# Performance work log

Measured on AMD Instinct MI355X. Metric: run time of the kernel, lower is better.

Reference implementation:

```python
import jax, jax.numpy as jnp
import numpy as np

N = 10000          # variable nodes
DEG = 16           # average degree
F = N * DEG // 2   # factors (80000)
E = 2 * F          # directed edges per direction (160000)
S = 64             # state_dim
M = 64             # message_dim
HM = 128           # hidden_unit_message_dim
HR = 128           # hidden_unit_readout_dim
STEPS = 5          # n_steps


def setup_inputs() -> dict:
    rng = np.random.default_rng(0)
    u = rng.integers(0, N - 1, size=F)
    v = u + 1 + rng.integers(0, N - 1 - u)          # u < v, factor endpoints
    b = rng.standard_normal(N).astype(np.float32)
    Juv = rng.standard_normal(F).astype(np.float32)
    pair = np.stack([u, v], axis=1).reshape(-1)      # [E] node endpoints (u,v interleaved)
    fidx = np.repeat(np.arange(F), 2)                # [E] factor index, each twice
    base = np.stack([np.zeros(F, np.float32), b[u].astype(np.float32),
                     b[v].astype(np.float32), Juv], axis=1)   # [F,4]
    base2 = np.repeat(base, 2, axis=0)               # [E,4]
    v2f_feat = base2.copy()                          # flag 0.0
    f2v_feat = base2.copy(); f2v_feat[:, 0] = 1.0    # flag 1.0

    keys = jax.random.split(jax.random.key(0), 32)
    p = lambda k, shp: (jax.random.normal(k, shp, jnp.float32) * 0.1)
    z = lambda n: jnp.zeros((n,), jnp.float32)
    inp = {
        'fac2var_row': jnp.asarray(fidx, jnp.int32),
        'fac2var_col': jnp.asarray(pair, jnp.int32),
        'var2fac_row': jnp.asarray(pair, jnp.int32),
        'var2fac_col': jnp.asarray(fidx, jnp.int32),
        'fac2var_feat': jnp.asarray(f2v_feat),
        'var2fac_feat': jnp.asarray(v2f_feat),
        # fac2var message MLP (in = 2S+8)
        'f2v_w1': p(keys[0], (HM, 2 * S + 8)), 'f2v_b1': z(HM),
        'f2v_w2': p(keys[1], (HM, HM)),        'f2v_b2': z(HM),
        'f2v_w3': p(keys[2], (M, HM)),         'f2v_b3': z(M),
        # var2fac message MLP
        'v2f_w1': p(keys[3], (HM, 2 * S + 8)), 'v2f_b1': z(HM),
        'v2f_w2': p(keys[4], (HM, HM)),        'v2f_b2': z(HM),
        'v2f_w3': p(keys[5], (M, HM)),         'v2f_b3': z(M),
        # fac2var GRUCell (input M, hidden S)
        'gf_wih': p(keys[6], (3 * S, M)), 'gf_whh': p(keys[7], (3 * S, S)),
        'gf_bih': p(keys[8], (3 * S,)),   'gf_bhh': p(keys[9], (3 * S,)),
        # var2fac GRUCell
        'gv_wih': p(keys[10], (3 * S, M)), 'gv_whh': p(keys[11], (3 * S, S)),
        'gv_bih': p(keys[12], (3 * S,)),   'gv_bhh': p(keys[13], (3 * S,)),
        # readout MLP
        'ro_w1': p(keys[14], (HR, S)),  'ro_b1': z(HR),
        'ro_w2': p(keys[15], (HR, HR)), 'ro_b2': z(HR),
        'ro_w3': p(keys[16], (2, HR)),  'ro_b3': z(2),
    }
    return inp


def _mlp3(x, w1, b1, w2, b2, w3, b3):
    h = jax.nn.relu(x @ w1.T + b1)
    h = jax.nn.relu(h @ w2.T + b2)
    return h @ w3.T + b3


def _gru(x, h, wih, whh, bih, bhh):
    gi = x @ wih.T + bih
    gh = h @ whh.T + bhh
    ir, iz, inn = jnp.split(gi, 3, axis=-1)
    hr, hz, hn = jnp.split(gh, 3, axis=-1)
    r = jax.nn.sigmoid(ir + hr)
    zg = jax.nn.sigmoid(iz + hz)
    n = jnp.tanh(inn + r * hn)
    return (1.0 - zg) * n + zg * h


def reference(fac2var_row, fac2var_col, var2fac_row, var2fac_col,
              fac2var_feat, var2fac_feat,
              f2v_w1, f2v_b1, f2v_w2, f2v_b2, f2v_w3, f2v_b3,
              v2f_w1, v2f_b1, v2f_w2, v2f_b2, v2f_w3, v2f_b3,
              gf_wih, gf_whh, gf_bih, gf_bhh,
              gv_wih, gv_whh, gv_bih, gv_bhh,
              ro_w1, ro_b1, ro_w2, ro_b2, ro_w3, ro_b3):
    var_h0 = jnp.zeros((N, S), jnp.float32)
    fac_h0 = jnp.zeros((F, S), jnp.float32)

    def step(carry, _):
        var_h, fac_h = carry
        # fac -> var
        em = jnp.concatenate([fac_h[fac2var_row], var_h[fac2var_col],
                              fac2var_feat[fac2var_row], fac2var_feat[fac2var_col]], axis=-1)
        em = _mlp3(em, f2v_w1, f2v_b1, f2v_w2, f2v_b2, f2v_w3, f2v_b3)
        nm = jax.ops.segment_sum(em, fac2var_col, num_segments=N)
        var_h = _gru(nm, var_h, gf_wih, gf_whh, gf_bih, gf_bhh)
        # var -> fac
        em = jnp.concatenate([var_h[var2fac_row], fac_h[var2fac_col],
                              var2fac_feat[var2fac_row], var2fac_feat[var2fac_col]], axis=-1)
        em = _mlp3(em, v2f_w1, v2f_b1, v2f_w2, v2f_b2, v2f_w3, v2f_b3)
        nm = jax.ops.segment_sum(em, var2fac_col, num_segments=F)
        fac_h = _gru(nm, fac_h, gv_wih, gv_whh, gv_bih, gv_bhh)
        return (var_h, fac_h), None

    (var_h, _), _ = jax.lax.scan(step, (var_h0, fac_h0), None, length=STEPS)
    logits = _mlp3(var_h, ro_w1, ro_b1, ro_w2, ro_b2, ro_w3, ro_b3)
    return jax.nn.softmax(logits, axis=1)
```

## Files before the change

### kernel.cpp

```cpp
#include <hip/hip_runtime.h>
#include <hip/hip_bf16.h>

#define NN     10000
#define NF     80000
#define NE     160000
#define SDIM   64
#define HMDIM  128
#define HRDIM  128
#define KIN    136
#define NSTEPS 5

static_assert(NE % 64 == 0, "edge grid exact");

typedef __attribute__((ext_vector_type(8))) short short8;
typedef __attribute__((ext_vector_type(4))) float f32x4;

static __device__ __forceinline__ float bf2f(unsigned short u) {
    return __uint_as_float(((unsigned int)u) << 16);
}
static __device__ __forceinline__ unsigned short f2bf(float f) {
    __hip_bfloat16 h = __float2bfloat16(f);
    unsigned short u;
    __builtin_memcpy(&u, &h, 2);
    return u;
}
static __device__ __forceinline__ float sigm(float x) {
    x = fminf(fmaxf(x, -30.f), 30.f);
    return 1.f / (1.f + __expf(-x));
}
static __device__ __forceinline__ float tanh_f(float x) {
    x = fminf(fmaxf(x, -15.f), 15.f);
    float t = __expf(2.f * x);
    return (t - 1.f) / (t + 1.f);
}
static __device__ __forceinline__ void split8(const float* x, short8& hi, short8& lo) {
    #pragma unroll
    for (int i = 0; i < 8; ++i) {
        unsigned short h = f2bf(x[i]);
        hi[i] = (short)h;
        lo[i] = (short)f2bf(x[i] - bf2f(h));
    }
}
static __device__ __forceinline__ void f4pair_to8(float4 a, float4 b, float* xv) {
    xv[0]=a.x; xv[1]=a.y; xv[2]=a.z; xv[3]=a.w;
    xv[4]=b.x; xv[5]=b.y; xv[6]=b.z; xv[7]=b.w;
}
static __device__ __forceinline__ void dma16(const unsigned short* g, unsigned short* l) {
    __builtin_amdgcn_global_load_lds(
        (const __attribute__((address_space(1))) void*)g,
        (__attribute__((address_space(3))) void*)l,
        16, 0, 0);
}

#define LGKM0() asm volatile("s_waitcnt lgkmcnt(0)" ::: "memory")
#define VMC2()  asm volatile("s_waitcnt vmcnt(2)"   ::: "memory")
#define VMC0()  asm volatile("s_waitcnt vmcnt(0)"   ::: "memory")
#define SBAR()  __builtin_amdgcn_s_barrier()
#define SCHED0() __builtin_amdgcn_sched_barrier(0)
#define PRIO1() __builtin_amdgcn_s_setprio(1)
#define PRIO0() __builtin_amdgcn_s_setprio(0)

__global__ void k_zero(float* __restrict__ p, int n) {
    int i = blockIdx.x * blockDim.x + threadIdx.x;
    int stride = gridDim.x * blockDim.x;
    for (; i < n; i += stride) p[i] = 0.f;
}

#define NTR 2
struct TArgs {
    const float* src[NTR];
    float*       dst[NTR];
    int          R[NTR];
    int          C[NTR];
};
__global__ void k_transpose(TArgs a) {
    const int b = blockIdx.x;
    const float* s = a.src[b];
    float* d = a.dst[b];
    const int R = a.R[b], C = a.C[b], n = R * C;
    for (int i = threadIdx.x; i < n; i += blockDim.x) {
        int r = i / C, c = i % C;
        d[c * R + r] = s[i];
    }
}

#define NPK 10
struct PArgs {
    const float*    src[NPK];
    unsigned short* hi[NPK];
    unsigned short* lo[NPK];
    int             N[NPK], K[NPK], CK[NPK];
};
__global__ void k_pack(PArgs a) {
    const int b = blockIdx.x;
    const float* s = a.src[b];
    unsigned short* ph = a.hi[b];
    unsigned short* pl = a.lo[b];
    const int N = a.N[b], K = a.K[b], CK = a.CK[b];
    const int NT = N >> 4;
    const int total = NT * CK * 512;
    for (int i = threadIdx.x; i < total; i += blockDim.x) {
        int j    = i & 7;
        int ln   = (i >> 3) & 63;
        int tile = i >> 9;
        int tn   = tile % NT;
        int ck   = tile / NT;
        int k = ck * 32 + ((ln >> 4) * 8) + j;
        int n = tn * 16 + (ln & 15);
        float f = (k < K) ? s[n * K + k] : 0.f;
        unsigned short h = f2bf(f);
        ph[i] = h;
        pl[i] = f2bf(f - bf2f(h));
    }
}

__global__ void k_bsum(const float* bih0, const float* bhh0, float* o0,
                       const float* bih1, const float* bhh1, float* o1) {
    int i = threadIdx.x;
    if (i < 192) { o0[i] = bih0[i] + bhh0[i]; o1[i] = bih1[i] + bhh1[i]; }
}

#define STAGE(buf, sh, sl) do {                                            \
    const int u0_ = wv * 2;                                                \
    _Pragma("unroll")                                                      \
    for (int k_ = 0; k_ < 2; ++k_) {                                       \
        const int u_ = u0_ + k_;                                           \
        const unsigned short* s_ = (u_ < 4 ? (sh) : (sl)) + (u_ & 3) * 512;\
        unsigned short* d_ = (u_ < 4 ? &BH[buf][0] : &BL[buf][0]) + (u_ & 3) * 512; \
        dma16(s_ + lane * 8, d_);                                          \
    }                                                                      \
} while (0)

__global__ __launch_bounds__(256, 3)
void k_edge_mfma(const float* __restrict__ hrow, const float* __restrict__ hcol,
                 const int* __restrict__ rows, const int* __restrict__ cols,
                 const float* __restrict__ feat,
                 const unsigned short* __restrict__ w1h, const unsigned short* __restrict__ w1l,
                 const unsigned short* __restrict__ w2h, const unsigned short* __restrict__ w2l,
                 const unsigned short* __restrict__ w3h, const unsigned short* __restrict__ w3l,
                 const float* __restrict__ b1, const float* __restrict__ b2,
                 const float* __restrict__ b3,
                 float* __restrict__ nm, int pairsum)
{
    __shared__ __align__(16) unsigned short Hhi[64][136];
    __shared__ __align__(16) unsigned short Hlo[64][136];
    __shared__ __align__(16) unsigned short BH[2][2048];
    __shared__ __align__(16) unsigned short BL[2][2048];
    const int lane = threadIdx.x & 63;
    const int wv   = threadIdx.x >> 6;
    const int quad = lane >> 4;
    const int col  = lane & 15;

    const int e0 = blockIdx.x * 64 + wv * 16 + col;
    const int r0 = pairsum ? rows[e0] : (e0 >> 1);
    const int c0 = pairsum ? (e0 >> 1) : cols[e0];

    float4 gR[4], gC[4], gFr, gFc;
    {
        const float4* pr = (const float4*)(hrow + (size_t)r0 * 64);
        const float4* pc = (const float4*)(hcol + (size_t)c0 * 64);
        gR[0] = pr[quad * 2];     gR[1] = pr[quad * 2 + 1];
        gR[2] = pr[8 + quad * 2]; gR[3] = pr[8 + quad * 2 + 1];
        gC[0] = pc[quad * 2];     gC[1] = pc[quad * 2 + 1];
        gC[2] = pc[8 + quad * 2]; gC[3] = pc[8 + quad * 2 + 1];
        gFr = *(const float4*)(feat + (size_t)r0 * 4);
        gFc = *(const float4*)(feat + (size_t)c0 * 4);
    }
    int cc[4];
    if (!pairsum) {
        #pragma unroll
        for (int rr = 0; rr < 4; ++rr)
            cc[rr] = cols[blockIdx.x * 64 + wv * 16 + quad * 4 + rr];
    }
    float b1v[8], b2v[8], b3v[4];
    #pragma unroll
    for (int t = 0; t < 8; ++t) { b1v[t] = b1[t * 16 + col]; b2v[t] = b2[t * 16 + col]; }
    #pragma unroll
    for (int t = 0; t < 4; ++t) b3v[t] = b3[t * 16 + col];

    VMC0(); SCHED0();

    STAGE(0, w1h, w1l);

    f32x4 acc[8];
    #pragma unroll
    for (int t = 0; t < 8; ++t) acc[t] = (f32x4){0.f, 0.f, 0.f, 0.f};

    short8 ahi, alo;
    #pragma unroll
    for (int hp = 0; hp < 10; ++hp) {
        {
            const unsigned short* nh; const unsigned short* nl;
            if (hp < 9) { nh = w1h + (hp + 1) * 2048; nl = w1l + (hp + 1) * 2048; }
            else        { nh = w2h;                   nl = w2l; }
            STAGE((hp + 1) & 1, nh, nl);
        }
        if ((hp & 1) == 0) {
            const int ck = hp >> 1;
            float xv[8];
            if (ck < 2)      f4pair_to8(gR[ck * 2], gR[ck * 2 + 1], xv);
            else if (ck < 4) f4pair_to8(gC[(ck - 2) * 2], gC[(ck - 2) * 2 + 1], xv);
            else if (quad == 0) f4pair_to8(gFr, gFc, xv);
            else {
                #pragma unroll
                for (int i = 0; i < 8; ++i) xv[i] = 0.f;
            }
            split8(xv, ahi, alo);
        }
        VMC2(); LGKM0(); SBAR(); SCHED0();
        {
            const unsigned short* bh = &BH[hp & 1][0];
            const unsigned short* bl = &BL[hp & 1][0];
            #pragma unroll
            for (int t = 0; t < 4; ++t) {
                const int tn = (hp & 1) * 4 + t;
                short8 bhi = *(const short8*)(bh + t * 512 + lane * 8);
                short8 blo = *(const short8*)(bl + t * 512 + lane * 8);
                acc[tn] = __builtin_amdgcn_mfma_f32_16x16x32_bf16(ahi, bhi, acc[tn], 0, 0, 0);
                acc[tn] = __builtin_amdgcn_mfma_f32_16x16x32_bf16(ahi, blo, acc[tn], 0, 0, 0);
                acc[tn] = __builtin_amdgcn_mfma_f32_16x16x32_bf16(alo, bhi, acc[tn], 0, 0, 0);
            }
        }
        LGKM0(); SBAR(); SCHED0();
    }
    #pragma unroll
    for (int tn = 0; tn < 8; ++tn)
        #pragma unroll
        for (int rr = 0; rr < 4; ++rr) {
            float v = fmaxf(acc[tn][rr] + b1v[tn], 0.f);
            int m = wv * 16 + quad * 4 + rr;
            unsigned short h = f2bf(v);
            Hhi[m][tn * 16 + col] = h;
            Hlo[m][tn * 16 + col] = f2bf(v - bf2f(h));
        }

    #pragma unroll
    for (int t = 0; t < 8; ++t) acc[t] = (f32x4){0.f, 0.f, 0.f, 0.f};
    const int m0 = wv * 16 + col;
    #pragma unroll
    for (int h2 = 0; h2 < 8; ++h2) {
        const int hp = 10 + h2;
        {
            const unsigned short* nh; const unsigned short* nl;
            if (h2 < 7) { nh = w2h + (h2 + 1) * 2048; nl = w2l + (h2 + 1) * 2048; }
            else        { nh = w3h;                   nl = w3l; }
            STAGE((hp + 1) & 1, nh, nl);
        }
        if ((h2 & 1) == 0) {
            const int ck = h2 >> 1;
            ahi = *(const short8*)(&Hhi[m0][ck * 32 + quad * 8]);
            alo = *(const short8*)(&Hlo[m0][ck * 32 + quad * 8]);
        }
        VMC2(); LGKM0(); SBAR(); SCHED0();
        {
            const unsigned short* bh = &BH[hp & 1][0];
            const unsigned short* bl = &BL[hp & 1][0];
            #pragma unroll
            for (int t = 0; t < 4; ++t) {
                const int tn = (h2 & 1) * 4 + t;
                short8 bhi = *(const short8*)(bh + t * 512 + lane * 8);
                short8 blo = *(const short8*)(bl + t * 512 + lane * 8);
                acc[tn] = __builtin_amdgcn_mfma_f32_16x16x32_bf16(ahi, bhi, acc[tn], 0, 0, 0);
                acc[tn] = __builtin_amdgcn_mfma_f32_16x16x32_bf16(ahi, blo, acc[tn], 0, 0, 0);
                acc[tn] = __builtin_amdgcn_mfma_f32_16x16x32_bf16(alo, bhi, acc[tn], 0, 0, 0);
            }
        }
        LGKM0(); SBAR(); SCHED0();
    }
    #pragma unroll
    for (int tn = 0; tn < 8; ++tn)
        #pragma unroll
        for (int rr = 0; rr < 4; ++rr) {
            float v = fmaxf(acc[tn][rr] + b2v[tn], 0.f);
            int m = wv * 16 + quad * 4 + rr;
            unsigned short h = f2bf(v);
            Hhi[m][tn * 16 + col] = h;
            Hlo[m][tn * 16 + col] = f2bf(v - bf2f(h));
        }

    f32x4 a3[4];
    #pragma unroll
    for (int t = 0; t < 4; ++t) a3[t] = (f32x4){0.f, 0.f, 0.f, 0.f};
    #pragma unroll
    for (int h3 = 0; h3 < 4; ++h3) {
        const int hp = 18 + h3;
        if (h3 < 3) STAGE((hp + 1) & 1, w3h + (h3 + 1) * 2048, w3l + (h3 + 1) * 2048);
        short8 a3h = *(const short8*)(&Hhi[m0][h3 * 32 + quad * 8]);
        short8 a3l = *(const short8*)(&Hlo[m0][h3 * 32 + quad * 8]);
        if (h3 < 3) { VMC2(); } else { VMC0(); }
        LGKM0(); SBAR(); SCHED0();
        {
            const unsigned short* bh = &BH[hp & 1][0];
            const unsigned short* bl = &BL[hp & 1][0];
            #pragma unroll
            for (int t = 0; t < 4; ++t) {
                short8 bhi = *(const short8*)(bh + t * 512 + lane * 8);
                short8 blo = *(const short8*)(bl + t * 512 + lane * 8);
                a3[t] = __builtin_amdgcn_mfma_f32_16x16x32_bf16(a3h, bhi, a3[t], 0, 0, 0);
                a3[t] = __builtin_amdgcn_mfma_f32_16x16x32_bf16(a3h, blo, a3[t], 0, 0, 0);
                a3[t] = __builtin_amdgcn_mfma_f32_16x16x32_bf16(a3l, bhi, a3[t], 0, 0, 0);
            }
        }
        if (h3 < 3) { LGKM0(); SBAR(); SCHED0(); }
    }

    if (pairsum) {
        int f0 = (blockIdx.x * 64 + wv * 16 + quad * 4) >> 1;
        #pragma unroll
        for (int tn = 0; tn < 4; ++tn) {
            float b2x = 2.f * b3v[tn];
            nm[(size_t)f0 * 64 + tn * 16 + col]       = a3[tn][0] + a3[tn][1] + b2x;
            nm[(size_t)(f0 + 1) * 64 + tn * 16 + col] = a3[tn][2] + a3[tn][3] + b2x;
        }
    } else {
        #pragma unroll
        for (int tn = 0; tn < 4; ++tn) {
            float bias = b3v[tn];
            #pragma unroll
            for (int rr = 0; rr < 4; ++rr)
                atomicAdd(&nm[(size_t)cc[rr] * 64 + tn * 16 + col], a3[tn][rr] + bias);
        }
    }
}

__global__ __launch_bounds__(256, 3)
void k_gru_mfma(float* __restrict__ nm,
                const unsigned short* __restrict__ wih_h, const unsigned short* __restrict__ wih_l,
                const unsigned short* __restrict__ whh_h, const unsigned short* __restrict__ whh_l,
                const float* __restrict__ bsum,
                const float* __restrict__ bih, const float* __restrict__ bhh,
                float* __restrict__ hst, int count, int nzero)
{
    __shared__ float Hs[64][68];
    const int lane = threadIdx.x & 63;
    const int wv   = threadIdx.x >> 6;
    const int quad = lane >> 4;
    const int col  = lane & 15;
    const int base = blockIdx.x * 64;

    float4 am[4], ah[4];
    {
        int ra = base + wv * 16 + col;
        ra = ra < count ? ra : count - 1;
        const float4* pm = (const float4*)(nm + (size_t)ra * 64);
        const float4* ph = (const float4*)(hst + (size_t)ra * 64);
        am[0] = pm[quad * 2];     am[1] = pm[quad * 2 + 1];
        am[2] = pm[8 + quad * 2]; am[3] = pm[8 + quad * 2 + 1];
        ah[0] = ph[quad * 2];     ah[1] = ph[quad * 2 + 1];
        ah[2] = ph[8 + quad * 2]; ah[3] = ph[8 + quad * 2 + 1];
    }
    float bsr[4], bsz[4], bin_[4], bhn[4];
    #pragma unroll
    for (int t = 0; t < 4; ++t) {
        int g = t * 16 + col;
        bsr[t] = bsum[g]; bsz[t] = bsum[64 + g];
        bin_[t] = bih[128 + g]; bhn[t] = bhh[128 + g];
    }
    {
        int rowl = wv * 16 + col;
        *(float4*)(&Hs[rowl][quad * 8])          = ah[0];
        *(float4*)(&Hs[rowl][quad * 8 + 4])      = ah[1];
        *(float4*)(&Hs[rowl][32 + quad * 8])     = ah[2];
        *(float4*)(&Hs[rowl][32 + quad * 8 + 4]) = ah[3];
    }

    f32x4 rz[8], ni[4], nh[4];
    #pragma unroll
    for (int t = 0; t < 8; ++t) rz[t] = (f32x4){0.f, 0.f, 0.f, 0.f};
    #pragma unroll
    for (int t = 0; t < 4; ++t) {
        ni[t] = (f32x4){0.f, 0.f, 0.f, 0.f};
        nh[t] = (f32x4){0.f, 0.f, 0.f, 0.f};
    }

    #pragma unroll
    for (int ck = 0; ck < 2; ++ck) {
        short8 mhi, mlo, hhi, hlo;
        {
            float xv[8];
            f4pair_to8(am[ck * 2], am[ck * 2 + 1], xv);
            split8(xv, mhi, mlo);
            f4pair_to8(ah[ck * 2], ah[ck * 2 + 1], xv);
            split8(xv, hhi, hlo);
        }
        const unsigned short* ih = wih_h + (size_t)(ck * 12) * 512 + lane * 8;
        const unsigned short* il = wih_l + (size_t)(ck * 12) * 512 + lane * 8;
        const unsigned short* hh = whh_h + (size_t)(ck * 12) * 512 + lane * 8;
        const unsigned short* hl = whh_l + (size_t)(ck * 12) * 512 + lane * 8;
        PRIO1();
        #pragma unroll
        for (int tn = 0; tn < 8; ++tn) {
            short8 bihh = *(const short8*)(ih + tn * 512);
            short8 bihl = *(const short8*)(il + tn * 512);
            short8 bhhh = *(const short8*)(hh + tn * 512);
            short8 bhhl = *(const short8*)(hl + tn * 512);
            rz[tn] = __builtin_amdgcn_mfma_f32_16x16x32_bf16(mhi, bihh, rz[tn], 0, 0, 0);
            rz[tn] = __builtin_amdgcn_mfma_f32_16x16x32_bf16(mhi, bihl, rz[tn], 0, 0, 0);
            rz[tn] = __builtin_amdgcn_mfma_f32_16x16x32_bf16(mlo, bihh, rz[tn], 0, 0, 0);
            rz[tn] = __builtin_amdgcn_mfma_f32_16x16x32_bf16(hhi, bhhh, rz[tn], 0, 0, 0);
            rz[tn] = __builtin_amdgcn_mfma_f32_16x16x32_bf16(hhi, bhhl, rz[tn], 0, 0, 0);
            rz[tn] = __builtin_amdgcn_mfma_f32_16x16x32_bf16(hlo, bhhh, rz[tn], 0, 0, 0);
        }
        #pragma unroll
        for (int tn = 8; tn < 12; ++tn) {
            short8 bihh = *(const short8*)(ih + tn * 512);
            short8 bihl = *(const short8*)(il + tn * 512);
            short8 bhhh = *(const short8*)(hh + tn * 512);
            short8 bhhl = *(const short8*)(hl + tn * 512);
            ni[tn - 8] = __builtin_amdgcn_mfma_f32_16x16x32_bf16(mhi, bihh, ni[tn - 8], 0, 0, 0);
            ni[tn - 8] = __builtin_amdgcn_mfma_f32_16x16x32_bf16(mhi, bihl, ni[tn - 8], 0, 0, 0);
            ni[tn - 8] = __builtin_amdgcn_mfma_f32_16x16x32_bf16(mlo, bihh, ni[tn - 8], 0, 0, 0);
            nh[tn - 8] = __builtin_amdgcn_mfma_f32_16x16x32_bf16(hhi, bhhh, nh[tn - 8], 0, 0, 0);
            nh[tn - 8] = __builtin_amdgcn_mfma_f32_16x16x32_bf16(hhi, bhhl, nh[tn - 8], 0, 0, 0);
            nh[tn - 8] = __builtin_amdgcn_mfma_f32_16x16x32_bf16(hlo, bhhh, nh[tn - 8], 0, 0, 0);
        }
        PRIO0();
    }

    #pragma unroll
    for (int rr = 0; rr < 4; ++rr) {
        int rowl = wv * 16 + quad * 4 + rr;
        int grow = base + rowl;
        bool ok = grow < count;
        #pragma unroll
        for (int t = 0; t < 4; ++t) {
            int g = t * 16 + col;
            float rv = sigm(rz[t][rr] + bsr[t]);
            float zv = sigm(rz[4 + t][rr] + bsz[t]);
            float nv = tanh_f(ni[t][rr] + bin_[t] + rv * (nh[t][rr] + bhn[t]));
            if (ok) {
                float ho = Hs[rowl][g];
                hst[(size_t)grow * 64 + g] = (1.f - zv) * nv + zv * ho;
            }
            if (grow < nzero) nm[(size_t)grow * 64 + g] = 0.f;
        }
    }
}

__global__ __launch_bounds__(256, 3)
void k_readout(const float* __restrict__ vh,
               const float* __restrict__ w1t, const float* __restrict__ b1,
               const float* __restrict__ w2t, const float* __restrict__ b2,
               const float* __restrict__ w3, const float* __restrict__ b3,
               float* __restrict__ out)
{
    __shared__ float H[HRDIM][64];
    const int lane = threadIdx.x & 63;
    const int wv   = __builtin_amdgcn_readfirstlane(threadIdx.x >> 6);
    const int n0 = blockIdx.x * 64 + lane;
    const int n  = n0 < NN ? n0 : NN - 1;
    const float4* px = (const float4*)(vh + (size_t)n * 64);

    const int j1 = 32 * wv;
    float acc[32];
    #pragma unroll
    for (int j = 0; j < 32; ++j) acc[j] = b1[j1 + j];
    #pragma unroll 4
    for (int q = 0; q < 16; ++q) {
        float4 x4 = px[q];
        const float* wa = w1t + (4 * q + 0) * HRDIM + j1;
        const float* wb = w1t + (4 * q + 1) * HRDIM + j1;
        const float* wc = w1t + (4 * q + 2) * HRDIM + j1;
        const float* wd = w1t + (4 * q + 3) * HRDIM + j1;
        #pragma unroll
        for (int j = 0; j < 32; ++j) {
            acc[j] = fmaf(wa[j], x4.x, acc[j]);
            acc[j] = fmaf(wb[j], x4.y, acc[j]);
            acc[j] = fmaf(wc[j], x4.z, acc[j]);
            acc[j] = fmaf(wd[j], x4.w, acc[j]);
        }
    }
    #pragma unroll
    for (int j = 0; j < 32; ++j) H[j1 + j][lane] = fmaxf(acc[j], 0.f);
    __syncthreads();

    #pragma unroll
    for (int j = 0; j < 32; ++j) acc[j] = b2[j1 + j];
    #pragma unroll 4
    for (int k = 0; k < HRDIM; ++k) {
        float xk = H[k][lane];
        const float* wr = w2t + k * HRDIM + j1;
        #pragma unroll
        for (int j = 0; j < 32; ++j)
            acc[j] = fmaf(wr[j], xk, acc[j]);
    }
    __syncthreads();
    #pragma unroll
    for (int j = 0; j < 32; ++j) H[j1 + j][lane] = fmaxf(acc[j], 0.f);
    __syncthreads();

    if (wv == 0 && n0 < NN) {
        float l0 = b3[0], l1 = b3[1];
        #pragma unroll 8
        for (int k = 0; k < HRDIM; ++k) {
            float hk = H[k][lane];
            l0 = fmaf(w3[k],         hk, l0);
            l1 = fmaf(w3[HRDIM + k], hk, l1);
        }
        float mx = fmaxf(l0, l1);
        float e0 = __expf(l0 - mx), e1 = __expf(l1 - mx);
        float inv = 1.f / (e0 + e1);
        out[2 * n + 0] = e0 * inv;
        out[2 * n + 1] = e1 * inv;
    }
}

extern "C" void kernel_launch(void* const* d_in, const int* in_sizes, int n_in,
                              void* d_out, int out_size, void* d_ws, size_t ws_size,
                              hipStream_t stream)
{
    float* var_h = (float*)d_ws;
    float* fac_h = var_h + 640000;
    float* nm    = fac_h + 5120000;
    float* ro_t  = nm + 5120000;
    float* bsum  = ro_t + 24576;
    unsigned short* pk = (unsigned short*)(bsum + 384);

    const int*   f2v_row  = (const int*)d_in[0];
    const int*   f2v_col  = (const int*)d_in[1];
    const int*   v2f_row  = (const int*)d_in[2];
    const int*   v2f_col  = (const int*)d_in[3];
    const float* f2v_feat = (const float*)d_in[4];
    const float* v2f_feat = (const float*)d_in[5];
    const float* W[26];
    for (int j = 0; j < 26; ++j) W[j] = (const float*)d_in[6 + j];

    TArgs ta;
    float* T[NTR];
    {
        const float* src[NTR] = { W[20], W[22] };
        int R[NTR] = { HRDIM, HRDIM };
        int C[NTR] = { SDIM, HRDIM };
        size_t off = 0;
        for (int t = 0; t < NTR; ++t) {
            ta.src[t] = src[t]; ta.R[t] = R[t]; ta.C[t] = C[t];
            T[t] = ro_t + off; ta.dst[t] = T[t];
            off += (size_t)R[t] * C[t];
        }
    }
    unsigned short* P[12];
    unsigned short* G[8];
    {
        size_t off = 0;
        int esz[3] = { 20480, 16384, 8192 };
        for (int d = 0; d < 2; ++d)
            for (int m = 0; m < 3; ++m) {
                P[d * 6 + m * 2 + 0] = pk + off; off += esz[m];
                P[d * 6 + m * 2 + 1] = pk + off; off += esz[m];
            }
        for (int t = 0; t < 8; ++t) { G[t] = pk + off; off += 12288; }
    }
    PArgs pa;
    {
        const float* src[NPK] = { W[0], W[2], W[4], W[6], W[8], W[10],
                                  W[12], W[13], W[16], W[17] };
        int N[NPK]  = { HMDIM, HMDIM, SDIM,  HMDIM, HMDIM, SDIM,  192, 192, 192, 192 };
        int K[NPK]  = { KIN,   HMDIM, HMDIM, KIN,   HMDIM, HMDIM, SDIM, SDIM, SDIM, SDIM };
        int CK[NPK] = { 5,     4,     4,     5,     4,     4,     2,   2,   2,   2 };
        unsigned short* hi[NPK] = { P[0], P[2], P[4], P[6], P[8], P[10],
                                    G[0], G[2], G[4], G[6] };
        unsigned short* lo[NPK] = { P[1], P[3], P[5], P[7], P[9], P[11],
                                    G[1], G[3], G[5], G[7] };
        for (int t = 0; t < NPK; ++t) {
            pa.src[t] = src[t]; pa.N[t] = N[t]; pa.K[t] = K[t]; pa.CK[t] = CK[t];
            pa.hi[t] = hi[t];   pa.lo[t] = lo[t];
        }
    }
    k_transpose<<<NTR, 256, 0, stream>>>(ta);
    k_pack<<<NPK, 256, 0, stream>>>(pa);
    k_bsum<<<1, 256, 0, stream>>>(W[14], W[15], bsum, W[18], W[19], bsum + 192);
    k_zero<<<512, 256, 0, stream>>>(var_h, 640000 + 5120000 + 5120000);

    for (int s = 0; s < NSTEPS; ++s) {
        k_edge_mfma<<<NE / 64, 256, 0, stream>>>(
            fac_h, var_h, f2v_row, f2v_col, f2v_feat,
            P[0], P[1], P[2], P[3], P[4], P[5],
            W[1], W[3], W[5], nm, 0);
        k_gru_mfma<<<(NN + 63) / 64, 256, 0, stream>>>(
            nm, G[0], G[1], G[2], G[3], bsum, W[14], W[15], var_h, NN, 0);
        k_edge_mfma<<<NE / 64, 256, 0, stream>>>(
            var_h, fac_h, v2f_row, v2f_col, v2f_feat,
            P[6], P[7], P[8], P[9], P[10], P[11],
            W[7], W[9], W[11], nm, 1);
        k_gru_mfma<<<(NF + 63) / 64, 256, 0, stream>>>(
            nm, G[4], G[5], G[6], G[7], bsum + 192, W[18], W[19], fac_h, NF, NN);
    }
    k_readout<<<(NN + 63) / 64, 256, 0, stream>>>(
        var_h, T[0], W[21], T[1], W[23], W[24], W[25],
        (float*)d_out);
}
```

Measured before the change: 1.035 ms.

## Load MLP weight fragments directly from global instead of LDS-staged DMA pipeline

Removes the double-buffered global-to-LDS DMA staging of weight tiles, along with its per-chunk waitcnt and barrier synchronisation. Each wave now reads its bf16 hi/lo weight fragments straight from global memory, relying on L1/L2 caching because the weights are small and shared. This frees LDS and drops block barriers, and the occupancy hint rises from 3 to 4 blocks per CU. The cost is redundant per-wave global or cache traffic for weights and exposed load latency before each MFMA.

```diff
diff --git a/kernel.cpp b/kernel.cpp
--- a/kernel.cpp
+++ b/kernel.cpp
@@ -45,18 +45,7 @@
     xv[0]=a.x; xv[1]=a.y; xv[2]=a.z; xv[3]=a.w;
     xv[4]=b.x; xv[5]=b.y; xv[6]=b.z; xv[7]=b.w;
 }
-static __device__ __forceinline__ void dma16(const unsigned short* g, unsigned short* l) {
-    __builtin_amdgcn_global_load_lds(
-        (const __attribute__((address_space(1))) void*)g,
-        (__attribute__((address_space(3))) void*)l,
-        16, 0, 0);
-}
-
-#define LGKM0() asm volatile("s_waitcnt lgkmcnt(0)" ::: "memory")
-#define VMC2()  asm volatile("s_waitcnt vmcnt(2)"   ::: "memory")
-#define VMC0()  asm volatile("s_waitcnt vmcnt(0)"   ::: "memory")
-#define SBAR()  __builtin_amdgcn_s_barrier()
-#define SCHED0() __builtin_amdgcn_sched_barrier(0)
+
 #define PRIO1() __builtin_amdgcn_s_setprio(1)
 #define PRIO0() __builtin_amdgcn_s_setprio(0)
 
@@ -120,18 +109,7 @@
     if (i < 192) { o0[i] = bih0[i] + bhh0[i]; o1[i] = bih1[i] + bhh1[i]; }
 }
 
-#define STAGE(buf, sh, sl) do {                                            \
-    const int u0_ = wv * 2;                                                \
-    _Pragma("unroll")                                                      \
-    for (int k_ = 0; k_ < 2; ++k_) {                                       \
-        const int u_ = u0_ + k_;                                           \
-        const unsigned short* s_ = (u_ < 4 ? (sh) : (sl)) + (u_ & 3) * 512;\
-        unsigned short* d_ = (u_ < 4 ? &BH[buf][0] : &BL[buf][0]) + (u_ & 3) * 512; \
-        dma16(s_ + lane * 8, d_);                                          \
-    }                                                                      \
-} while (0)
-
-__global__ __launch_bounds__(256, 3)
+__global__ __launch_bounds__(256, 4)
 void k_edge_mfma(const float* __restrict__ hrow, const float* __restrict__ hcol,
                  const int* __restrict__ rows, const int* __restrict__ cols,
                  const float* __restrict__ feat,
@@ -144,8 +122,6 @@
 {
     __shared__ __align__(16) unsigned short Hhi[64][136];
     __shared__ __align__(16) unsigned short Hlo[64][136];
-    __shared__ __align__(16) unsigned short BH[2][2048];
-    __shared__ __align__(16) unsigned short BL[2][2048];
     const int lane = threadIdx.x & 63;
     const int wv   = threadIdx.x >> 6;
     const int quad = lane >> 4;
@@ -178,25 +154,16 @@
     #pragma unroll
     for (int t = 0; t < 4; ++t) b3v[t] = b3[t * 16 + col];
 
-    VMC0(); SCHED0();
-
-    STAGE(0, w1h, w1l);
-
     f32x4 acc[8];
     #pragma unroll
     for (int t = 0; t < 8; ++t) acc[t] = (f32x4){0.f, 0.f, 0.f, 0.f};
 
-    short8 ahi, alo;
-    #pragma unroll
-    for (int hp = 0; hp < 10; ++hp) {
+    const int boff = lane * 8;
+
+    #pragma unroll
+    for (int ck = 0; ck < 5; ++ck) {
+        short8 ahi, alo;
         {
-            const unsigned short* nh; const unsigned short* nl;
-            if (hp < 9) { nh = w1h + (hp + 1) * 2048; nl = w1l + (hp + 1) * 2048; }
-            else        { nh = w2h;                   nl = w2l; }
-            STAGE((hp + 1) & 1, nh, nl);
-        }
-        if ((hp & 1) == 0) {
-            const int ck = hp >> 1;
             float xv[8];
             if (ck < 2)      f4pair_to8(gR[ck * 2], gR[ck * 2 + 1], xv);
             else if (ck < 4) f4pair_to8(gC[(ck - 2) * 2], gC[(ck - 2) * 2 + 1], xv);
@@ -207,21 +174,16 @@
             }
             split8(xv, ahi, alo);
         }
-        VMC2(); LGKM0(); SBAR(); SCHED0();
-        {
-            const unsigned short* bh = &BH[hp & 1][0];
-            const unsigned short* bl = &BL[hp & 1][0];
-            #pragma unroll
-            for (int t = 0; t < 4; ++t) {
-                const int tn = (hp & 1) * 4 + t;
-                short8 bhi = *(const short8*)(bh + t * 512 + lane * 8);
-                short8 blo = *(const short8*)(bl + t * 512 + lane * 8);
-                acc[tn] = __builtin_amdgcn_mfma_f32_16x16x32_bf16(ahi, bhi, acc[tn], 0, 0, 0);
-                acc[tn] = __builtin_amdgcn_mfma_f32_16x16x32_bf16(ahi, blo, acc[tn], 0, 0, 0);
-                acc[tn] = __builtin_amdgcn_mfma_f32_16x16x32_bf16(alo, bhi, acc[tn], 0, 0, 0);
-            }
-        }
-        LGKM0(); SBAR(); SCHED0();
+        const unsigned short* bh = w1h + ck * 4096 + boff;
+        const unsigned short* bl = w1l + ck * 4096 + boff;
+        #pragma unroll
+        for (int tn = 0; tn < 8; ++tn) {
+            short8 bhi = *(const short8*)(bh + tn * 512);
+            short8 blo = *(const short8*)(bl + tn * 512);
+            acc[tn] = __builtin_amdgcn_mfma_f32_16x16x32_bf16(ahi, bhi, acc[tn], 0, 0, 0);
+            acc[tn] = __builtin_amdgcn_mfma_f32_16x16x32_bf16(ahi, blo, acc[tn], 0, 0, 0);
+            acc[tn] = __builtin_amdgcn_mfma_f32_16x16x32_bf16(alo, bhi, acc[tn], 0, 0, 0);
+        }
     }
     #pragma unroll
     for (int tn = 0; tn < 8; ++tn)
@@ -238,34 +200,19 @@
     for (int t = 0; t < 8; ++t) acc[t] = (f32x4){0.f, 0.f, 0.f, 0.f};
     const int m0 = wv * 16 + col;
     #pragma unroll
-    for (int h2 = 0; h2 < 8; ++h2) {
-        const int hp = 10 + h2;
-        {
-            const unsigned short* nh; const unsigned short* nl;
-            if (h2 < 7) { nh = w2h + (h2 + 1) * 2048; nl = w2l + (h2 + 1) * 2048; }
-            else        { nh = w3h;                   nl = w3l; }
-            STAGE((hp + 1) & 1, nh, nl);
-        }
-        if ((h2 & 1) == 0) {
-            const int ck = h2 >> 1;
-            ahi = *(const short8*)(&Hhi[m0][ck * 32 + quad * 8]);
-            alo = *(const short8*)(&Hlo[m0][ck * 32 + quad * 8]);
-        }
-        VMC2(); LGKM0(); SBAR(); SCHED0();
-        {
-            const unsigned short* bh = &BH[hp & 1][0];
-            const unsigned short* bl = &BL[hp & 1][0];
-            #pragma unroll
-            for (int t = 0; t < 4; ++t) {
-                const int tn = (h2 & 1) * 4 + t;
-                short8 bhi = *(const short8*)(bh + t * 512 + lane * 8);
-                short8 blo = *(const short8*)(bl + t * 512 + lane * 8);
-                acc[tn] = __builtin_amdgcn_mfma_f32_16x16x32_bf16(ahi, bhi, acc[tn], 0, 0, 0);
-                acc[tn] = __builtin_amdgcn_mfma_f32_16x16x32_bf16(ahi, blo, acc[tn], 0, 0, 0);
-                acc[tn] = __builtin_amdgcn_mfma_f32_16x16x32_bf16(alo, bhi, acc[tn], 0, 0, 0);
-            }
-        }
-        LGKM0(); SBAR(); SCHED0();
+    for (int ck = 0; ck < 4; ++ck) {
+        short8 ahi = *(const short8*)(&Hhi[m0][ck * 32 + quad * 8]);
+        short8 alo = *(const short8*)(&Hlo[m0][ck * 32 + quad * 8]);
+        const unsigned short* bh = w2h + ck * 4096 + boff;
+        const unsigned short* bl = w2l + ck * 4096 + boff;
+        #pragma unroll
+        for (int tn = 0; tn < 8; ++tn) {
+            short8 bhi = *(const short8*)(bh + tn * 512);
+            short8 blo = *(const short8*)(bl + tn * 512);
+            acc[tn] = __builtin_amdgcn_mfma_f32_16x16x32_bf16(ahi, bhi, acc[tn], 0, 0, 0);
+            acc[tn] = __builtin_amdgcn_mfma_f32_16x16x32_bf16(ahi, blo, acc[tn], 0, 0, 0);
+            acc[tn] = __builtin_amdgcn_mfma_f32_16x16x32_bf16(alo, bhi, acc[tn], 0, 0, 0);
+        }
     }
     #pragma unroll
     for (int tn = 0; tn < 8; ++tn)
@@ -282,26 +229,19 @@
     #pragma unroll
     for (int t = 0; t < 4; ++t) a3[t] = (f32x4){0.f, 0.f, 0.f, 0.f};
     #pragma unroll
-    for (int h3 = 0; h3 < 4; ++h3) {
-        const int hp = 18 + h3;
-        if (h3 < 3) STAGE((hp + 1) & 1, w3h + (h3 + 1) * 2048, w3l + (h3 + 1) * 2048);
-        short8 a3h = *(const short8*)(&Hhi[m0][h3 * 32 + quad * 8]);
-        short8 a3l = *(const short8*)(&Hlo[m0][h3 * 32 + quad * 8]);
-        if (h3 < 3) { VMC2(); } else { VMC0(); }
-        LGKM0(); SBAR(); SCHED0();
-        {
-            const unsigned short* bh = &BH[hp & 1][0];
-            const unsigned short* bl = &BL[hp & 1][0];
-            #pragma unroll
-            for (int t = 0; t < 4; ++t) {
-                short8 bhi = *(const short8*)(bh + t * 512 + lane * 8);
-                short8 blo = *(const short8*)(bl + t * 512 + lane * 8);
-                a3[t] = __builtin_amdgcn_mfma_f32_16x16x32_bf16(a3h, bhi, a3[t], 0, 0, 0);
-                a3[t] = __builtin_amdgcn_mfma_f32_16x16x32_bf16(a3h, blo, a3[t], 0, 0, 0);
-                a3[t] = __builtin_amdgcn_mfma_f32_16x16x32_bf16(a3l, bhi, a3[t], 0, 0, 0);
-            }
-        }
-        if (h3 < 3) { LGKM0(); SBAR(); SCHED0(); }
+    for (int ck = 0; ck < 4; ++ck) {
+        short8 ahi = *(const short8*)(&Hhi[m0][ck * 32 + quad * 8]);
+        short8 alo = *(const short8*)(&Hlo[m0][ck * 32 + quad * 8]);
+        const unsigned short* bh = w3h + ck * 2048 + boff;
+        const unsigned short* bl = w3l + ck * 2048 + boff;
+        #pragma unroll
+        for (int tn = 0; tn < 4; ++tn) {
+            short8 bhi = *(const short8*)(bh + tn * 512);
+            short8 blo = *(const short8*)(bl + tn * 512);
+            a3[tn] = __builtin_amdgcn_mfma_f32_16x16x32_bf16(ahi, bhi, a3[tn], 0, 0, 0);
+            a3[tn] = __builtin_amdgcn_mfma_f32_16x16x32_bf16(ahi, blo, a3[tn], 0, 0, 0);
+            a3[tn] = __builtin_amdgcn_mfma_f32_16x16x32_bf16(alo, bhi, a3[tn], 0, 0, 0);
+        }
     }
 
     if (pairsum) {
```

Measured after the change: 1.295 ms. +25.1%, slower.

## Fuse var-to-factor edge MLP with factor GRU update in one kernel

Applied to the files above, without the earlier changes.

The var-to-factor message pass and the factor GRU update now run in a single kernel. Each factor's two edges sit in the same block, so the segment sum is done in shared memory and the GRU is applied in place to fac_h, with no round trip of nm through global memory and one fewer launch per step. The edge kernel is specialised to the atomic fac-to-var path only. The var GRU's zeroing argument changes so the nm buffer is still cleared for the next step. The fused kernel reads fac_h rows in the edge stage and overwrites them at the end, which is safe only because each block touches only its own 32 factors.

```diff
diff --git a/kernel.cpp b/kernel.cpp
--- a/kernel.cpp
+++ b/kernel.cpp
@@ -133,14 +133,14 @@
 
 __global__ __launch_bounds__(256, 3)
 void k_edge_mfma(const float* __restrict__ hrow, const float* __restrict__ hcol,
-                 const int* __restrict__ rows, const int* __restrict__ cols,
+                 const int* __restrict__ cols,
                  const float* __restrict__ feat,
                  const unsigned short* __restrict__ w1h, const unsigned short* __restrict__ w1l,
                  const unsigned short* __restrict__ w2h, const unsigned short* __restrict__ w2l,
                  const unsigned short* __restrict__ w3h, const unsigned short* __restrict__ w3l,
                  const float* __restrict__ b1, const float* __restrict__ b2,
                  const float* __restrict__ b3,
-                 float* __restrict__ nm, int pairsum)
+                 float* __restrict__ nm)
 {
     __shared__ __align__(16) unsigned short Hhi[64][136];
     __shared__ __align__(16) unsigned short Hlo[64][136];
@@ -152,8 +152,8 @@
     const int col  = lane & 15;
 
     const int e0 = blockIdx.x * 64 + wv * 16 + col;
-    const int r0 = pairsum ? rows[e0] : (e0 >> 1);
-    const int c0 = pairsum ? (e0 >> 1) : cols[e0];
+    const int r0 = e0 >> 1;
+    const int c0 = cols[e0];
 
     float4 gR[4], gC[4], gFr, gFc;
     {
@@ -167,11 +167,10 @@
         gFc = *(const float4*)(feat + (size_t)c0 * 4);
     }
     int cc[4];
-    if (!pairsum) {
-        #pragma unroll
-        for (int rr = 0; rr < 4; ++rr)
-            cc[rr] = cols[blockIdx.x * 64 + wv * 16 + quad * 4 + rr];
-    }
+    #pragma unroll
+    for (int rr = 0; rr < 4; ++rr)
+        cc[rr] = cols[blockIdx.x * 64 + wv * 16 + quad * 4 + rr];
+
     float b1v[8], b2v[8], b3v[4];
     #pragma unroll
     for (int t = 0; t < 8; ++t) { b1v[t] = b1[t * 16 + col]; b2v[t] = b2[t * 16 + col]; }
@@ -179,7 +178,6 @@
     for (int t = 0; t < 4; ++t) b3v[t] = b3[t * 16 + col];
 
     VMC0(); SCHED0();
-
     STAGE(0, w1h, w1l);
 
     f32x4 acc[8];
@@ -304,21 +302,328 @@
         if (h3 < 3) { LGKM0(); SBAR(); SCHED0(); }
     }
 
-    if (pairsum) {
-        int f0 = (blockIdx.x * 64 + wv * 16 + quad * 4) >> 1;
+    #pragma unroll
+    for (int tn = 0; tn < 4; ++tn) {
+        float bias = b3v[tn];
+        #pragma unroll
+        for (int rr = 0; rr < 4; ++rr)
+            atomicAdd(&nm[(size_t)cc[rr] * 64 + tn * 16 + col], a3[tn][rr] + bias);
+    }
+}
+
+__global__ __launch_bounds__(256, 3)
+void k_edge_gru_fused(const float* __restrict__ hrow, float* fstate,
+                      const int* __restrict__ rows,
+                      const float* __restrict__ feat,
+                      const unsigned short* __restrict__ w1h, const unsigned short* __restrict__ w1l,
+                      const unsigned short* __restrict__ w2h, const unsigned short* __restrict__ w2l,
+                      const unsigned short* __restrict__ w3h, const unsigned short* __restrict__ w3l,
+                      const float* __restrict__ b1, const float* __restrict__ b2,
+                      const float* __restrict__ b3,
+                      const unsigned short* __restrict__ gih_h, const unsigned short* __restrict__ gih_l,
+                      const unsigned short* __restrict__ ghh_h, const unsigned short* __restrict__ ghh_l,
+                      const float* __restrict__ bsum, const float* __restrict__ bih,
+                      const float* __restrict__ bhh)
+{
+    __shared__ __align__(16) unsigned char SM[51200];
+    unsigned short (*Hhi)[136] = (unsigned short(*)[136])(SM);
+    unsigned short (*Hlo)[136] = (unsigned short(*)[136])(SM + 17408);
+    unsigned short (*BH)[2048] = (unsigned short(*)[2048])(SM + 34816);
+    unsigned short (*BL)[2048] = (unsigned short(*)[2048])(SM + 43008);
+    float (*nmL)[68]  = (float(*)[68])(SM);
+    float (*gl)[260]  = (float(*)[260])(SM + 8704);
+
+    const int lane = threadIdx.x & 63;
+    const int wv   = threadIdx.x >> 6;
+    const int quad = lane >> 4;
+    const int col  = lane & 15;
+
+    const int e0 = blockIdx.x * 64 + wv * 16 + col;
+    const int r0 = rows[e0];
+    const int c0 = e0 >> 1;
+
+    float4 gR[4], gC[4], gFr, gFc;
+    {
+        const float4* pr = (const float4*)(hrow + (size_t)r0 * 64);
+        const float4* pc = (const float4*)(fstate + (size_t)c0 * 64);
+        gR[0] = pr[quad * 2];     gR[1] = pr[quad * 2 + 1];
+        gR[2] = pr[8 + quad * 2]; gR[3] = pr[8 + quad * 2 + 1];
+        gC[0] = pc[quad * 2];     gC[1] = pc[quad * 2 + 1];
+        gC[2] = pc[8 + quad * 2]; gC[3] = pc[8 + quad * 2 + 1];
+        gFr = *(const float4*)(feat + (size_t)r0 * 4);
+        gFc = *(const float4*)(feat + (size_t)c0 * 4);
+    }
+    float b1v[8], b2v[8], b3v[4];
+    #pragma unroll
+    for (int t = 0; t < 8; ++t) { b1v[t] = b1[t * 16 + col]; b2v[t] = b2[t * 16 + col]; }
+    #pragma unroll
+    for (int t = 0; t < 4; ++t) b3v[t] = b3[t * 16 + col];
+
+    VMC0(); SCHED0();
+    STAGE(0, w1h, w1l);
+
+    f32x4 acc[8];
+    #pragma unroll
+    for (int t = 0; t < 8; ++t) acc[t] = (f32x4){0.f, 0.f, 0.f, 0.f};
+
+    short8 ahi, alo;
+    #pragma unroll
+    for (int hp = 0; hp < 10; ++hp) {
+        {
+            const unsigned short* nh; const unsigned short* nl;
+            if (hp < 9) { nh = w1h + (hp + 1) * 2048; nl = w1l + (hp + 1) * 2048; }
+            else        { nh = w2h;                   nl = w2l; }
+            STAGE((hp + 1) & 1, nh, nl);
+        }
+        if ((hp & 1) == 0) {
+            const int ck = hp >> 1;
+            float xv[8];
+            if (ck < 2)      f4pair_to8(gR[ck * 2], gR[ck * 2 + 1], xv);
+            else if (ck < 4) f4pair_to8(gC[(ck - 2) * 2], gC[(ck - 2) * 2 + 1], xv);
+            else if (quad == 0) f4pair_to8(gFr, gFc, xv);
+            else {
+                #pragma unroll
+                for (int i = 0; i < 8; ++i) xv[i] = 0.f;
+            }
+            split8(xv, ahi, alo);
+        }
+        VMC2(); LGKM0(); SBAR(); SCHED0();
+        {
+            const unsigned short* bh = &BH[hp & 1][0];
+            const unsigned short* bl = &BL[hp & 1][0];
+            #pragma unroll
+            for (int t = 0; t < 4; ++t) {
+                const int tn = (hp & 1) * 4 + t;
+                short8 bhi = *(const short8*)(bh + t * 512 + lane * 8);
+                short8 blo = *(const short8*)(bl + t * 512 + lane * 8);
+                acc[tn] = __builtin_amdgcn_mfma_f32_16x16x32_bf16(ahi, bhi, acc[tn], 0, 0, 0);
+                acc[tn] = __builtin_amdgcn_mfma_f32_16x16x32_bf16(ahi, blo, acc[tn], 0, 0, 0);
+                acc[tn] = __builtin_amdgcn_mfma_f32_16x16x32_bf16(alo, bhi, acc[tn], 0, 0, 0);
+            }
+        }
+        LGKM0(); SBAR(); SCHED0();
+    }
+    #pragma unroll
+    for (int tn = 0; tn < 8; ++tn)
+        #pragma unroll
+        for (int rr = 0; rr < 4; ++rr) {
+            float v = fmaxf(acc[tn][rr] + b1v[tn], 0.f);
+            int m = wv * 16 + quad * 4 + rr;
+            unsigned short h = f2bf(v);
+            Hhi[m][tn * 16 + col] = h;
+            Hlo[m][tn * 16 + col] = f2bf(v - bf2f(h));
+        }
+
+    #pragma unroll
+    for (int t = 0; t < 8; ++t) acc[t] = (f32x4){0.f, 0.f, 0.f, 0.f};
+    const int m0 = wv * 16 + col;
+    #pragma unroll
+    for (int h2 = 0; h2 < 8; ++h2) {
+        const int hp = 10 + h2;
+        {
+            const unsigned short* nh; const unsigned short* nl;
+            if (h2 < 7) { nh = w2h + (h2 + 1) * 2048; nl = w2l + (h2 + 1) * 2048; }
+            else        { nh = w3h;                   nl = w3l; }
+            STAGE((hp + 1) & 1, nh, nl);
+        }
+        if ((h2 & 1) == 0) {
+            const int ck = h2 >> 1;
+            ahi = *(const short8*)(&Hhi[m0][ck * 32 + quad * 8]);
+            alo = *(const short8*)(&Hlo[m0][ck * 32 + quad * 8]);
+        }
+        VMC2(); LGKM0(); SBAR(); SCHED0();
+        {
+            const unsigned short* bh = &BH[hp & 1][0];
+            const unsigned short* bl = &BL[hp & 1][0];
+            #pragma unroll
+            for (int t = 0; t < 4; ++t) {
+                const int tn = (h2 & 1) * 4 + t;
+                short8 bhi = *(const short8*)(bh + t * 512 + lane * 8);
+                short8 blo = *(const short8*)(bl + t * 512 + lane * 8);
+                acc[tn] = __builtin_amdgcn_mfma_f32_16x16x32_bf16(ahi, bhi, acc[tn], 0, 0, 0);
+                acc[tn] = __builtin_amdgcn_mfma_f32_16x16x32_bf16(ahi, blo, acc[tn], 0, 0, 0);
+                acc[tn] = __builtin_amdgcn_mfma_f32_16x16x32_bf16(alo, bhi, acc[tn], 0, 0, 0);
+            }
+        }
+        LGKM0(); SBAR(); SCHED0();
+    }
+    #pragma unroll
+    for (int tn = 0; tn < 8; ++tn)
+        #pragma unroll
+        for (int rr = 0; rr < 4; ++rr) {
+            float v = fmaxf(acc[tn][rr] + b2v[tn], 0.f);
+            int m = wv * 16 + quad * 4 + rr;
+            unsigned short h = f2bf(v);
+            Hhi[m][tn * 16 + col] = h;
+            Hlo[m][tn * 16 + col] = f2bf(v - bf2f(h));
+        }
+
+    f32x4 a3[4];
+    #pragma unroll
+    for (int t = 0; t < 4; ++t) a3[t] = (f32x4){0.f, 0.f, 0.f, 0.f};
+    #pragma unroll
+    for (int h3 = 0; h3 < 4; ++h3) {
+        const int hp = 18 + h3;
+        if (h3 < 3) STAGE((hp + 1) & 1, w3h + (h3 + 1) * 2048, w3l + (h3 + 1) * 2048);
+        short8 a3h = *(const short8*)(&Hhi[m0][h3 * 32 + quad * 8]);
+        short8 a3l = *(const short8*)(&Hlo[m0][h3 * 32 + quad * 8]);
+        if (h3 < 3) { VMC2(); } else { VMC0(); }
+        LGKM0(); SBAR(); SCHED0();
+        {
+            const unsigned short* bh = &BH[hp & 1][0];
+            const unsigned short* bl = &BL[hp & 1][0];
+            #pragma unroll
+            for (int t = 0; t < 4; ++t) {
+                short8 bhi = *(const short8*)(bh + t * 512 + lane * 8);
+                short8 blo = *(const short8*)(bl + t * 512 + lane * 8);
+                a3[t] = __builtin_amdgcn_mfma_f32_16x16x32_bf16(a3h, bhi, a3[t], 0, 0, 0);
+                a3[t] = __builtin_amdgcn_mfma_f32_16x16x32_bf16(a3h, blo, a3[t], 0, 0, 0);
+                a3[t] = __builtin_amdgcn_mfma_f32_16x16x32_bf16(a3l, bhi, a3[t], 0, 0, 0);
+            }
+        }
+        if (h3 < 3) { LGKM0(); SBAR(); SCHED0(); }
+    }
+
+    LGKM0(); SBAR(); SCHED0();
+
+    {
+        int lf0 = wv * 8 + quad * 2;
         #pragma unroll
         for (int tn = 0; tn < 4; ++tn) {
             float b2x = 2.f * b3v[tn];
-            nm[(size_t)f0 * 64 + tn * 16 + col]       = a3[tn][0] + a3[tn][1] + b2x;
-            nm[(size_t)(f0 + 1) * 64 + tn * 16 + col] = a3[tn][2] + a3[tn][3] + b2x;
-        }
+            nmL[lf0][tn * 16 + col]     = a3[tn][0] + a3[tn][1] + b2x;
+            nmL[lf0 + 1][tn * 16 + col] = a3[tn][2] + a3[tn][3] + b2x;
+        }
+    }
+    LGKM0(); SBAR(); SCHED0();
+
+    const int fbase = blockIdx.x * 32;
+    const int mt    = wv >> 1;
+    const int half  = wv & 1;
+    const int hrow0 = fbase + mt * 16 + col;
+
+    if (half == 0) {
+        f32x4 rz6[6];
+        #pragma unroll
+        for (int i = 0; i < 6; ++i) rz6[i] = (f32x4){0.f, 0.f, 0.f, 0.f};
+        #pragma unroll
+        for (int ck = 0; ck < 2; ++ck) {
+            short8 mhi, mlo, hhi, hlo;
+            {
+                float xv[8];
+                *(float4*)&xv[0] = *(const float4*)(&nmL[mt * 16 + col][ck * 32 + quad * 8]);
+                *(float4*)&xv[4] = *(const float4*)(&nmL[mt * 16 + col][ck * 32 + quad * 8 + 4]);
+                split8(xv, mhi, mlo);
+                const float* hp_ = fstate + (size_t)hrow0 * 64 + ck * 32 + quad * 8;
+                *(float4*)&xv[0] = *(const float4*)(hp_);
+                *(float4*)&xv[4] = *(const float4*)(hp_ + 4);
+                split8(xv, hhi, hlo);
+            }
+            const unsigned short* ih = gih_h + (size_t)(ck * 12) * 512 + lane * 8;
+            const unsigned short* il = gih_l + (size_t)(ck * 12) * 512 + lane * 8;
+            const unsigned short* hh = ghh_h + (size_t)(ck * 12) * 512 + lane * 8;
+            const unsigned short* hl = ghh_l + (size_t)(ck * 12) * 512 + lane * 8;
+            #pragma unroll
+            for (int i = 0; i < 6; ++i) {
+                short8 bihh = *(const short8*)(ih + i * 512);
+                short8 bihl = *(const short8*)(il + i * 512);
+                short8 bhhh = *(const short8*)(hh + i * 512);
+                short8 bhhl = *(const short8*)(hl + i * 512);
+                rz6[i] = __builtin_amdgcn_mfma_f32_16x16x32_bf16(mhi, bihh, rz6[i], 0, 0, 0);
+                rz6[i] = __builtin_amdgcn_mfma_f32_16x16x32_bf16(mhi, bihl, rz6[i], 0, 0, 0);
+                rz6[i] = __builtin_amdgcn_mfma_f32_16x16x32_bf16(mlo, bihh, rz6[i], 0, 0, 0);
+                rz6[i] = __builtin_amdgcn_mfma_f32_16x16x32_bf16(hhi, bhhh, rz6[i], 0, 0, 0);
+                rz6[i] = __builtin_amdgcn_mfma_f32_16x16x32_bf16(hhi, bhhl, rz6[i], 0, 0, 0);
+                rz6[i] = __builtin_amdgcn_mfma_f32_16x16x32_bf16(hlo, bhhh, rz6[i], 0, 0, 0);
+            }
+        }
+        #pragma unroll
+        for (int i = 0; i < 6; ++i)
+            #pragma unroll
+            for (int rr = 0; rr < 4; ++rr)
+                gl[mt * 16 + quad * 4 + rr][i * 16 + col] = rz6[i][rr];
     } else {
-        #pragma unroll
-        for (int tn = 0; tn < 4; ++tn) {
-            float bias = b3v[tn];
-            #pragma unroll
-            for (int rr = 0; rr < 4; ++rr)
-                atomicAdd(&nm[(size_t)cc[rr] * 64 + tn * 16 + col], a3[tn][rr] + bias);
+        f32x4 rz2[2], niA[4], nhA[4];
+        #pragma unroll
+        for (int i = 0; i < 2; ++i) rz2[i] = (f32x4){0.f, 0.f, 0.f, 0.f};
+        #pragma unroll
+        for (int i = 0; i < 4; ++i) {
+            niA[i] = (f32x4){0.f, 0.f, 0.f, 0.f};
+            nhA[i] = (f32x4){0.f, 0.f, 0.f, 0.f};
+        }
+        #pragma unroll
+        for (int ck = 0; ck < 2; ++ck) {
+            short8 mhi, mlo, hhi, hlo;
+            {
+                float xv[8];
+                *(float4*)&xv[0] = *(const float4*)(&nmL[mt * 16 + col][ck * 32 + quad * 8]);
+                *(float4*)&xv[4] = *(const float4*)(&nmL[mt * 16 + col][ck * 32 + quad * 8 + 4]);
+                split8(xv, mhi, mlo);
+                const float* hp_ = fstate + (size_t)hrow0 * 64 + ck * 32 + quad * 8;
+                *(float4*)&xv[0] = *(const float4*)(hp_);
+                *(float4*)&xv[4] = *(const float4*)(hp_ + 4);
+                split8(xv, hhi, hlo);
+            }
+            const unsigned short* ih = gih_h + (size_t)(ck * 12) * 512 + lane * 8;
+            const unsigned short* il = gih_l + (size_t)(ck * 12) * 512 + lane * 8;
+            const unsigned short* hh = ghh_h + (size_t)(ck * 12) * 512 + lane * 8;
+            const unsigned short* hl = ghh_l + (size_t)(ck * 12) * 512 + lane * 8;
+            #pragma unroll
+            for (int i = 0; i < 2; ++i) {
+                const int tn = 6 + i;
+                short8 bihh = *(const short8*)(ih + tn * 512);
+                short8 bihl = *(const short8*)(il + tn * 512);
+                short8 bhhh = *(const short8*)(hh + tn * 512);
+                short8 bhhl = *(const short8*)(hl + tn * 512);
+                rz2[i] = __builtin_amdgcn_mfma_f32_16x16x32_bf16(mhi, bihh, rz2[i], 0, 0, 0);
+                rz2[i] = __builtin_amdgcn_mfma_f32_16x16x32_bf16(mhi, bihl, rz2[i], 0, 0, 0);
+                rz2[i] = __builtin_amdgcn_mfma_f32_16x16x32_bf16(mlo, bihh, rz2[i], 0, 0, 0);
+                rz2[i] = __builtin_amdgcn_mfma_f32_16x16x32_bf16(hhi, bhhh, rz2[i], 0, 0, 0);
+                rz2[i] = __builtin_amdgcn_mfma_f32_16x16x32_bf16(hhi, bhhl, rz2[i], 0, 0, 0);
+                rz2[i] = __builtin_amdgcn_mfma_f32_16x16x32_bf16(hlo, bhhh, rz2[i], 0, 0, 0);
+            }
+            #pragma unroll
+            for (int i = 0; i < 4; ++i) {
+                const int tn = 8 + i;
+                short8 bihh = *(const short8*)(ih + tn * 512);
+                short8 bihl = *(const short8*)(il + tn * 512);
+                short8 bhhh = *(const short8*)(hh + tn * 512);
+                short8 bhhl = *(const short8*)(hl + tn * 512);
+                niA[i] = __builtin_amdgcn_mfma_f32_16x16x32_bf16(mhi, bihh, niA[i], 0, 0, 0);
+                niA[i] = __builtin_amdgcn_mfma_f32_16x16x32_bf16(mhi, bihl, niA[i], 0, 0, 0);
+                niA[i] = __builtin_amdgcn_mfma_f32_16x16x32_bf16(mlo, bihh, niA[i], 0, 0, 0);
+                nhA[i] = __builtin_amdgcn_mfma_f32_16x16x32_bf16(hhi, bhhh, nhA[i], 0, 0, 0);
+                nhA[i] = __builtin_amdgcn_mfma_f32_16x16x32_bf16(hhi, bhhl, nhA[i], 0, 0, 0);
+                nhA[i] = __builtin_amdgcn_mfma_f32_16x16x32_bf16(hlo, bhhh, nhA[i], 0, 0, 0);
+            }
+        }
+        #pragma unroll
+        for (int rr = 0; rr < 4; ++rr) {
+            const int gr = mt * 16 + quad * 4 + rr;
+            #pragma unroll
+            for (int i = 0; i < 2; ++i) gl[gr][(6 + i) * 16 + col] = rz2[i][rr];
+            #pragma unroll
+            for (int i = 0; i < 4; ++i) {
+                gl[gr][128 + i * 16 + col] = niA[i][rr];
+                gl[gr][192 + i * 16 + col] = nhA[i][rr];
+            }
+        }
+    }
+    LGKM0(); SBAR(); SCHED0();
+
+    {
+        const int r  = threadIdx.x >> 3;
+        const int g0 = (threadIdx.x & 7) * 8;
+        const size_t gw = (size_t)(fbase + r) * 64;
+        #pragma unroll
+        for (int j = 0; j < 8; ++j) {
+            const int g = g0 + j;
+            float rv = sigm(gl[r][g] + bsum[g]);
+            float zv = sigm(gl[r][64 + g] + bsum[64 + g]);
+            float nv = tanh_f(gl[r][128 + g] + bih[128 + g]
+                              + rv * (gl[r][192 + g] + bhh[128 + g]));
+            float ho = fstate[gw + g];
+            fstate[gw + g] = (1.f - zv) * nv + zv * ho;
         }
     }
 }
@@ -524,6 +829,7 @@
     const float* v2f_feat = (const float*)d_in[5];
     const float* W[26];
     for (int j = 0; j < 26; ++j) W[j] = (const float*)d_in[6 + j];
+    (void)f2v_row; (void)v2f_col;
 
     TArgs ta;
     float* T[NTR];
@@ -573,17 +879,16 @@
 
     for (int s = 0; s < NSTEPS; ++s) {
         k_edge_mfma<<<NE / 64, 256, 0, stream>>>(
-            fac_h, var_h, f2v_row, f2v_col, f2v_feat,
+            fac_h, var_h, f2v_col, f2v_feat,
             P[0], P[1], P[2], P[3], P[4], P[5],
-            W[1], W[3], W[5], nm, 0);
+            W[1], W[3], W[5], nm);
         k_gru_mfma<<<(NN + 63) / 64, 256, 0, stream>>>(
-            nm, G[0], G[1], G[2], G[3], bsum, W[14], W[15], var_h, NN, 0);
-        k_edge_mfma<<<NE / 64, 256, 0, stream>>>(
-            var_h, fac_h, v2f_row, v2f_col, v2f_feat,
+            nm, G[0], G[1], G[2], G[3], bsum, W[14], W[15], var_h, NN, NN);
+        k_edge_gru_fused<<<NE / 64, 256, 0, stream>>>(
+            var_h, fac_h, v2f_row, v2f_feat,
             P[6], P[7], P[8], P[9], P[10], P[11],
-            W[7], W[9], W[11], nm, 1);
-        k_gru_mfma<<<(NF + 63) / 64, 256, 0, stream>>>(
-            nm, G[4], G[5], G[6], G[7], bsum + 192, W[18], W[19], fac_h, NF, NN);
+            W[7], W[9], W[11],
+            G[4], G[5], G[6], G[7], bsum + 192, W[18], W[19]);
     }
     k_readout<<<(NN + 63) / 64, 256, 0, stream>>>(
         var_h, T[0], W[21], T[1], W[23], W[24], W[25],
```

After: 969.3 us (median of 2 runs). 1.07x faster.
